# Kernel tuning notes

Hardware: AMD Instinct MI355X
Metric: run time of the kernel (lower is better)

## Reference

```python
import jax, jax.numpy as jnp
import numpy as np

OMEGA = 30.0

def _conv1x1(x, W, b):
    # x: [B, Cin, D, H, W]; W: [Cout, Cin]; b: [Cout]
    return jnp.einsum('oi,bidhw->bodhw', W, x) + b[None, :, None, None, None]

def setup_inputs() -> dict:
    key = jax.random.key(0)
    ks = jax.random.split(key, 12)
    B, D, H, Wd = 1, 8, 128, 128
    C = 256
    shp = (B, 3, D, H, Wd)
    std = np.sqrt(6.0 / C) / OMEGA
    return {
        'z': jax.random.normal(ks[0], shp, jnp.float32),
        'n': jax.random.normal(ks[1], shp, jnp.float32),
        'ad': jax.random.normal(ks[2], shp, jnp.float32),
        's': jax.random.normal(ks[3], shp, jnp.float32),
        'pixel_coords': jax.random.uniform(ks[4], shp, jnp.float32),
        'view_direction': jax.random.normal(ks[5], shp, jnp.float32),
        'W1': jax.random.normal(ks[6], (C, 12), jnp.float32) * std,
        'b1': jax.random.normal(ks[7], (C,), jnp.float32) * std,
        'W2': jax.random.normal(ks[8], (C, C), jnp.float32) * std,
        'b2': jax.random.normal(ks[9], (C,), jnp.float32) * std,
        'W4': jax.random.normal(ks[10], (3, C), jnp.float32) * 1e-4,
        'b4': jax.random.normal(ks[11], (3,), jnp.float32) * 1e-4,
    }

def reference(z, n, ad, s, pixel_coords, view_direction, W1, b1, W2, b2, W4, b4):
    # concat along channel dim: [B, 12, D, H, W]
    x = jnp.concatenate((s, n, pixel_coords, view_direction), axis=1)
    h = jnp.sin(OMEGA * _conv1x1(x, W1, b1))
    h = jnp.sin(OMEGA * _conv1x1(h, W2, b2))
    s_out = 0.5 * jnp.sin(OMEGA * _conv1x1(h, W4, b4))
    # lighting_predict_mode == 'total'
    return z + s_out
```

## Files before the change

kernel.cpp:

```cpp
#include <hip/hip_runtime.h>
#include <hip/hip_bf16.h>

#define NPIX (8*128*128)
#define CH   256
#define SCALE 4.774648292756860f

typedef __attribute__((ext_vector_type(8))) short bf16x8;
typedef __attribute__((ext_vector_type(4))) float f32x4;

__device__ inline unsigned int pkbf(float a, float b) {
    union { __hip_bfloat162 h; unsigned int u; } c;
    c.h = __float22bfloat162_rn(float2{a, b});
    return c.u;
}
__device__ inline unsigned short f2bf(float f) {
    unsigned int u = __float_as_uint(f);
    return (unsigned short)((u + 0x7FFFu + ((u >> 16) & 1u)) >> 16);
}
__device__ inline float sinrev(float t) {
    return __builtin_amdgcn_sinf(__builtin_amdgcn_fractf(t));
}
__device__ inline int kperm32(int k) {
    return (k & ~31) | ((k & 15) << 1) | ((k >> 4) & 1);
}

__global__ __launch_bounds__(256) void conv_weights(
    const float* __restrict__ W1, const float* __restrict__ W2,
    const float* __restrict__ W4,
    unsigned short* __restrict__ W2b, unsigned short* __restrict__ W1b,
    unsigned short* __restrict__ W4b)
{
    if (blockIdx.x < 256) {
        const int o = blockIdx.x, k = threadIdx.x;
        W2b[o*CH + kperm32(k)] = f2bf(W2[o*CH + k] * SCALE);
    } else {
        const int t = threadIdx.x;
        #pragma unroll
        for (int j = 0; j < 16; ++j)
            W1b[t*16 + j] = (j < 12) ? f2bf(W1[t*12 + j] * SCALE) : (unsigned short)0;
        const int kp = kperm32(t);
        #pragma unroll
        for (int r = 0; r < 16; ++r)
            W4b[r*CH + kp] = (r < 3) ? f2bf(W4[r*CH + t] * SCALE) : (unsigned short)0;
    }
}

template<bool PRE>
__global__ __launch_bounds__(512, 4) void rendernet5(
    const float* __restrict__ z,
    const float* __restrict__ nrm,
    const float* __restrict__ sph,
    const float* __restrict__ pc,
    const float* __restrict__ vd,
    const float* __restrict__ W1,
    const float* __restrict__ b1,
    const float* __restrict__ W2f,
    const unsigned short* __restrict__ W2b,
    const unsigned short* __restrict__ W1b,
    const float* __restrict__ b2,
    const float* __restrict__ W4f,
    const unsigned short* __restrict__ W4b,
    const float* __restrict__ b4,
    float* __restrict__ out)
{
    __shared__ __align__(16) char smem[64*512 + 64*80];
    char* xb = smem + 64*512;

    const int tid     = threadIdx.x;
    const int lane    = tid & 63;
    const int wave    = tid >> 6;
    const int lm      = lane & 15;
    const int lg      = lane >> 4;
    const int n0      = wave * 32;
    const int pixbase = blockIdx.x * 64;

    f32x4 acc[4][2];

    if constexpr (PRE) {
        {
            const int gp = pixbase + lane;
            unsigned int w0 = 0u, w1 = 0u;
            if (wave == 0) {
                w0 = pkbf(sph[0*NPIX+gp], sph[1*NPIX+gp]);
                w1 = pkbf(sph[2*NPIX+gp], nrm[0*NPIX+gp]);
            } else if (wave == 1) {
                w0 = pkbf(nrm[1*NPIX+gp], nrm[2*NPIX+gp]);
                w1 = pkbf(pc [0*NPIX+gp], pc [1*NPIX+gp]);
            } else if (wave == 2) {
                w0 = pkbf(pc[2*NPIX+gp], vd[0*NPIX+gp]);
                w1 = pkbf(vd[1*NPIX+gp], vd[2*NPIX+gp]);
            }
            *(unsigned int*)(xb + lane*80 + wave*8)     = w0;
            *(unsigned int*)(xb + lane*80 + wave*8 + 4) = w1;
        }
        __syncthreads();

        #pragma unroll
        for (int nf = 0; nf < 2; ++nf) {
            const float bv = b1[n0 + nf*16 + lm] * SCALE;
            #pragma unroll
            for (int mf = 0; mf < 4; ++mf) acc[mf][nf] = (f32x4){bv, bv, bv, bv};
        }

        bf16x8 w1f[2];
        #pragma unroll
        for (int nf = 0; nf < 2; ++nf) {
            bf16x8 t = *(const bf16x8*)(W1b + (n0 + nf*16 + lm)*16 + (lg & 1)*8);
            w1f[nf] = (lg < 2) ? t : (bf16x8){0,0,0,0,0,0,0,0};
        }
        bf16x8 ax[4];
        #pragma unroll
        for (int mf = 0; mf < 4; ++mf)
            ax[mf] = *(const bf16x8*)(xb + (mf*16 + lm)*80 + lg*16);

        #pragma unroll
        for (int nf = 0; nf < 2; ++nf)
            #pragma unroll
            for (int mf = 0; mf < 4; ++mf)
                acc[mf][nf] = __builtin_amdgcn_mfma_f32_16x16x32_bf16(
                                  ax[mf], w1f[nf], acc[mf][nf], 0, 0, 0);

        #pragma unroll
        for (int mf = 0; mf < 4; ++mf)
            #pragma unroll
            for (int r = 0; r < 4; ++r) {
                const int pix = mf*16 + lg*4 + r;
                const unsigned int pk = pkbf(sinrev(acc[mf][0][r]),
                                             sinrev(acc[mf][1][r]));
                *(unsigned int*)(smem + pix*512 + ((n0*2 + lm*4) ^ ((pix & 31) << 4))) = pk;
            }
    } else {
        const int gp = pixbase + lane;
        float xv[12];
        #pragma unroll
        for (int k = 0; k < 3; ++k) xv[k]     = sph[k*NPIX + gp];
        #pragma unroll
        for (int k = 0; k < 3; ++k) xv[3 + k] = nrm[k*NPIX + gp];
        #pragma unroll
        for (int k = 0; k < 3; ++k) xv[6 + k] = pc [k*NPIX + gp];
        #pragma unroll
        for (int k = 0; k < 3; ++k) xv[9 + k] = vd [k*NPIX + gp];
        #pragma unroll
        for (int c = 0; c < 32; ++c) {
            const int cc = n0 + c;
            float a = b1[cc];
            #pragma unroll
            for (int k = 0; k < 12; ++k) a += W1[cc*12 + k] * xv[k];
            const int kp = n0 + ((c & 15) << 1) + (c >> 4);
            *(unsigned short*)(smem + lane*512 + ((kp*2) ^ ((lane & 31) << 4))) =
                f2bf(__sinf(30.0f * a));
        }
    }
    __syncthreads();

    #pragma unroll
    for (int nf = 0; nf < 2; ++nf) {
        const float bv = PRE ? b2[n0 + nf*16 + lm] * SCALE : b2[n0 + nf*16 + lm];
        #pragma unroll
        for (int mf = 0; mf < 4; ++mf) acc[mf][nf] = (f32x4){bv, bv, bv, bv};
    }

    if constexpr (PRE) {
        const unsigned short* bp = W2b + (n0 + lm)*CH + lg*8;
        #pragma unroll
        for (int k0i = 0; k0i < 8; ++k0i) {
            bf16x8 bfr[2];
            #pragma unroll
            for (int nf = 0; nf < 2; ++nf)
                bfr[nf] = *(const bf16x8*)(bp + nf*16*CH + k0i*32);
            bf16x8 afr[4];
            #pragma unroll
            for (int mf = 0; mf < 4; ++mf) {
                const int pr = mf*16 + lm;
                afr[mf] = *(const bf16x8*)(smem + pr*512 +
                              ((k0i*64 + lg*16) ^ ((pr & 31) << 4)));
            }
            #pragma unroll
            for (int nf = 0; nf < 2; ++nf)
                #pragma unroll
                for (int mf = 0; mf < 4; ++mf)
                    acc[mf][nf] = __builtin_amdgcn_mfma_f32_16x16x32_bf16(
                                      afr[mf], bfr[nf], acc[mf][nf], 0, 0, 0);
        }
    } else {
        #pragma unroll
        for (int k0i = 0; k0i < 8; ++k0i) {
            bf16x8 afr[4];
            #pragma unroll
            for (int mf = 0; mf < 4; ++mf) {
                const int pr = mf*16 + lm;
                afr[mf] = *(const bf16x8*)(smem + pr*512 +
                              ((k0i*64 + lg*16) ^ ((pr & 31) << 4)));
            }
            #pragma unroll
            for (int nf = 0; nf < 2; ++nf) {
                bf16x8 t;
                #pragma unroll
                for (int j = 0; j < 8; ++j) {
                    const int kp = k0i*32 + lg*8 + j;
                    const int kr = (kp & ~31) | ((kp & 1) << 4) | ((kp >> 1) & 15);
                    t[j] = (short)f2bf(W2f[(n0 + nf*16 + lm)*CH + kr]);
                }
                #pragma unroll
                for (int mf = 0; mf < 4; ++mf)
                    acc[mf][nf] = __builtin_amdgcn_mfma_f32_16x16x32_bf16(
                                      afr[mf], t, acc[mf][nf], 0, 0, 0);
            }
        }
    }
    __syncthreads();

    #pragma unroll
    for (int mf = 0; mf < 4; ++mf)
        #pragma unroll
        for (int r = 0; r < 4; ++r) {
            const int pix = mf*16 + lg*4 + r;
            unsigned int pk;
            if constexpr (PRE)
                pk = pkbf(sinrev(acc[mf][0][r]), sinrev(acc[mf][1][r]));
            else
                pk = pkbf(__sinf(30.0f*acc[mf][0][r]), __sinf(30.0f*acc[mf][1][r]));
            *(unsigned int*)(smem + pix*512 + ((n0*2 + lm*4) ^ ((pix & 31) << 4))) = pk;
        }
    __syncthreads();

    if (wave == 0) {
        const float b4v = (lm < 3) ? (PRE ? b4[lm] * SCALE : b4[lm]) : 0.0f;
        f32x4 d[4];
        #pragma unroll
        for (int mf = 0; mf < 4; ++mf) d[mf] = (f32x4){b4v, b4v, b4v, b4v};

        #pragma unroll
        for (int k0i = 0; k0i < 8; ++k0i) {
            bf16x8 b4f;
            if constexpr (PRE) {
                b4f = *(const bf16x8*)(W4b + lm*CH + k0i*32 + lg*8);
            } else {
                #pragma unroll
                for (int j = 0; j < 8; ++j) {
                    const int kp = k0i*32 + lg*8 + j;
                    const int kr = (kp & ~31) | ((kp & 1) << 4) | ((kp >> 1) & 15);
                    b4f[j] = (lm < 3) ? (short)f2bf(W4f[lm*CH + kr]) : (short)0;
                }
            }
            bf16x8 afr[4];
            #pragma unroll
            for (int mf = 0; mf < 4; ++mf) {
                const int pr = mf*16 + lm;
                afr[mf] = *(const bf16x8*)(smem + pr*512 +
                              ((k0i*64 + lg*16) ^ ((pr & 31) << 4)));
            }
            #pragma unroll
            for (int mf = 0; mf < 4; ++mf)
                d[mf] = __builtin_amdgcn_mfma_f32_16x16x32_bf16(
                            afr[mf], b4f, d[mf], 0, 0, 0);
        }

        if (lm < 3) {
            #pragma unroll
            for (int mf = 0; mf < 4; ++mf)
                #pragma unroll
                for (int r = 0; r < 4; ++r) {
                    const int pix = mf*16 + lg*4 + r;
                    const int gi  = lm*NPIX + pixbase + pix;
                    const float sv = PRE ? sinrev(d[mf][r]) : __sinf(30.0f * d[mf][r]);
                    out[gi] = z[gi] + 0.5f * sv;
                }
        }
    }
}

extern "C" void kernel_launch(void* const* d_in, const int* in_sizes, int n_in,
                              void* d_out, int out_size, void* d_ws, size_t ws_size,
                              hipStream_t stream) {
    const float* z   = (const float*)d_in[0];
    const float* nrm = (const float*)d_in[1];
    const float* s   = (const float*)d_in[3];
    const float* pc  = (const float*)d_in[4];
    const float* vd  = (const float*)d_in[5];
    const float* W1  = (const float*)d_in[6];
    const float* b1  = (const float*)d_in[7];
    const float* W2  = (const float*)d_in[8];
    const float* b2  = (const float*)d_in[9];
    const float* W4  = (const float*)d_in[10];
    const float* b4  = (const float*)d_in[11];
    float* out = (float*)d_out;

    const size_t need = (size_t)(CH*CH + 16*CH + 16*CH) * sizeof(unsigned short);
    if (ws_size >= need) {
        unsigned short* W2b = (unsigned short*)d_ws;
        unsigned short* W1b = W2b + CH*CH;
        unsigned short* W4b = W1b + 16*CH;
        conv_weights<<<dim3(257), dim3(256), 0, stream>>>(W1, W2, W4, W2b, W1b, W4b);
        rendernet5<true><<<dim3(NPIX/64), dim3(512), 0, stream>>>(
            z, nrm, s, pc, vd, W1, b1, W2, W2b, W1b, b2, W4, W4b, b4, out);
    } else {
        rendernet5<false><<<dim3(NPIX/64), dim3(512), 0, stream>>>(
            z, nrm, s, pc, vd, W1, b1, W2, nullptr, nullptr, b2, W4, nullptr, b4, out);
    }
}
```

Baseline: 122.7 us.

## Widen block tile to 128 pixels with 2x4 wave grid over pixels and channels

Each block now handles 128 pixels instead of 64. The eight waves form a 2x4 grid, each computing a 64-pixel by 64-channel tile with 16 accumulators instead of 8. Every W2 fragment loaded from global memory now feeds twice as many MFMAs, which halves W2 traffic per pixel and the block count. In exchange, register pressure and LDS per block (about 74KB) both rise, which may reduce occupancy, and the final 3-channel projection now runs on two waves instead of one.

```diff
diff --git a/kernel.cpp b/kernel.cpp
--- a/kernel.cpp
+++ b/kernel.cpp
@@ -3,6 +3,7 @@
 
 #define NPIX (8*128*128)
 #define CH   256
+#define PPB  128
 #define SCALE 4.774648292756860f
 
 typedef __attribute__((ext_vector_type(8))) short bf16x8;
@@ -46,7 +47,7 @@
 }
 
 template<bool PRE>
-__global__ __launch_bounds__(512, 4) void rendernet5(
+__global__ __launch_bounds__(512, 4) void rendernet6(
     const float* __restrict__ z,
     const float* __restrict__ nrm,
     const float* __restrict__ sph,
@@ -63,58 +64,62 @@
     const float* __restrict__ b4,
     float* __restrict__ out)
 {
-    __shared__ __align__(16) char smem[64*512 + 64*80];
-    char* xb = smem + 64*512;
+    __shared__ __align__(16) char smem[PPB*512 + PPB*80];
+    char* xb = smem + PPB*512;
 
     const int tid     = threadIdx.x;
     const int lane    = tid & 63;
     const int wave    = tid >> 6;
+    const int wm      = wave >> 2;
+    const int wn      = wave & 3;
     const int lm      = lane & 15;
     const int lg      = lane >> 4;
-    const int n0      = wave * 32;
-    const int pixbase = blockIdx.x * 64;
-
-    f32x4 acc[4][2];
+    const int m0      = wm * 64;
+    const int n0      = wn * 64;
+    const int pixbase = blockIdx.x * PPB;
+
+    f32x4 acc[4][4];
 
     if constexpr (PRE) {
         {
-            const int gp = pixbase + lane;
-            unsigned int w0 = 0u, w1 = 0u;
-            if (wave == 0) {
-                w0 = pkbf(sph[0*NPIX+gp], sph[1*NPIX+gp]);
-                w1 = pkbf(sph[2*NPIX+gp], nrm[0*NPIX+gp]);
-            } else if (wave == 1) {
-                w0 = pkbf(nrm[1*NPIX+gp], nrm[2*NPIX+gp]);
-                w1 = pkbf(pc [0*NPIX+gp], pc [1*NPIX+gp]);
-            } else if (wave == 2) {
-                w0 = pkbf(pc[2*NPIX+gp], vd[0*NPIX+gp]);
-                w1 = pkbf(vd[1*NPIX+gp], vd[2*NPIX+gp]);
-            }
-            *(unsigned int*)(xb + lane*80 + wave*8)     = w0;
-            *(unsigned int*)(xb + lane*80 + wave*8 + 4) = w1;
+            const int p  = tid & 127;
+            const int sl = tid >> 7;
+            const int gp = pixbase + p;
+            union { unsigned int w[4]; bf16x8 v; } t;
+            t.w[0] = t.w[1] = t.w[2] = t.w[3] = 0u;
+            if (sl == 0) {
+                t.w[0] = pkbf(sph[0*NPIX+gp], sph[1*NPIX+gp]);
+                t.w[1] = pkbf(sph[2*NPIX+gp], nrm[0*NPIX+gp]);
+                t.w[2] = pkbf(nrm[1*NPIX+gp], nrm[2*NPIX+gp]);
+                t.w[3] = pkbf(pc [0*NPIX+gp], pc [1*NPIX+gp]);
+            } else if (sl == 1) {
+                t.w[0] = pkbf(pc[2*NPIX+gp], vd[0*NPIX+gp]);
+                t.w[1] = pkbf(vd[1*NPIX+gp], vd[2*NPIX+gp]);
+            }
+            *(bf16x8*)(xb + p*80 + sl*16) = t.v;
         }
         __syncthreads();
 
         #pragma unroll
-        for (int nf = 0; nf < 2; ++nf) {
+        for (int nf = 0; nf < 4; ++nf) {
             const float bv = b1[n0 + nf*16 + lm] * SCALE;
             #pragma unroll
             for (int mf = 0; mf < 4; ++mf) acc[mf][nf] = (f32x4){bv, bv, bv, bv};
         }
 
-        bf16x8 w1f[2];
-        #pragma unroll
-        for (int nf = 0; nf < 2; ++nf) {
+        bf16x8 w1f[4];
+        #pragma unroll
+        for (int nf = 0; nf < 4; ++nf) {
             bf16x8 t = *(const bf16x8*)(W1b + (n0 + nf*16 + lm)*16 + (lg & 1)*8);
             w1f[nf] = (lg < 2) ? t : (bf16x8){0,0,0,0,0,0,0,0};
         }
         bf16x8 ax[4];
         #pragma unroll
         for (int mf = 0; mf < 4; ++mf)
-            ax[mf] = *(const bf16x8*)(xb + (mf*16 + lm)*80 + lg*16);
-
-        #pragma unroll
-        for (int nf = 0; nf < 2; ++nf)
+            ax[mf] = *(const bf16x8*)(xb + (m0 + mf*16 + lm)*80 + lg*16);
+
+        #pragma unroll
+        for (int nf = 0; nf < 4; ++nf)
             #pragma unroll
             for (int mf = 0; mf < 4; ++mf)
                 acc[mf][nf] = __builtin_amdgcn_mfma_f32_16x16x32_bf16(
@@ -124,13 +129,17 @@
         for (int mf = 0; mf < 4; ++mf)
             #pragma unroll
             for (int r = 0; r < 4; ++r) {
-                const int pix = mf*16 + lg*4 + r;
-                const unsigned int pk = pkbf(sinrev(acc[mf][0][r]),
-                                             sinrev(acc[mf][1][r]));
-                *(unsigned int*)(smem + pix*512 + ((n0*2 + lm*4) ^ ((pix & 31) << 4))) = pk;
+                const int pix = m0 + mf*16 + lg*4 + r;
+                const int swz = (pix & 31) << 4;
+                *(unsigned int*)(smem + pix*512 + ((n0*2 + lm*4) ^ swz)) =
+                    pkbf(sinrev(acc[mf][0][r]), sinrev(acc[mf][1][r]));
+                *(unsigned int*)(smem + pix*512 + (((n0+32)*2 + lm*4) ^ swz)) =
+                    pkbf(sinrev(acc[mf][2][r]), sinrev(acc[mf][3][r]));
             }
     } else {
-        const int gp = pixbase + lane;
+        const int p  = tid & 127;
+        const int c0 = (tid >> 7) * 64;
+        const int gp = pixbase + p;
         float xv[12];
         #pragma unroll
         for (int k = 0; k < 3; ++k) xv[k]     = sph[k*NPIX + gp];
@@ -140,21 +149,20 @@
         for (int k = 0; k < 3; ++k) xv[6 + k] = pc [k*NPIX + gp];
         #pragma unroll
         for (int k = 0; k < 3; ++k) xv[9 + k] = vd [k*NPIX + gp];
-        #pragma unroll
-        for (int c = 0; c < 32; ++c) {
-            const int cc = n0 + c;
+        for (int c = 0; c < 64; ++c) {
+            const int cc = c0 + c;
             float a = b1[cc];
             #pragma unroll
             for (int k = 0; k < 12; ++k) a += W1[cc*12 + k] * xv[k];
-            const int kp = n0 + ((c & 15) << 1) + (c >> 4);
-            *(unsigned short*)(smem + lane*512 + ((kp*2) ^ ((lane & 31) << 4))) =
+            const int kp = kperm32(cc);
+            *(unsigned short*)(smem + p*512 + ((kp*2) ^ ((p & 31) << 4))) =
                 f2bf(__sinf(30.0f * a));
         }
     }
     __syncthreads();
 
     #pragma unroll
-    for (int nf = 0; nf < 2; ++nf) {
+    for (int nf = 0; nf < 4; ++nf) {
         const float bv = PRE ? b2[n0 + nf*16 + lm] * SCALE : b2[n0 + nf*16 + lm];
         #pragma unroll
         for (int mf = 0; mf < 4; ++mf) acc[mf][nf] = (f32x4){bv, bv, bv, bv};
@@ -164,19 +172,19 @@
         const unsigned short* bp = W2b + (n0 + lm)*CH + lg*8;
         #pragma unroll
         for (int k0i = 0; k0i < 8; ++k0i) {
-            bf16x8 bfr[2];
-            #pragma unroll
-            for (int nf = 0; nf < 2; ++nf)
+            bf16x8 bfr[4];
+            #pragma unroll
+            for (int nf = 0; nf < 4; ++nf)
                 bfr[nf] = *(const bf16x8*)(bp + nf*16*CH + k0i*32);
             bf16x8 afr[4];
             #pragma unroll
             for (int mf = 0; mf < 4; ++mf) {
-                const int pr = mf*16 + lm;
+                const int pr = m0 + mf*16 + lm;
                 afr[mf] = *(const bf16x8*)(smem + pr*512 +
                               ((k0i*64 + lg*16) ^ ((pr & 31) << 4)));
             }
             #pragma unroll
-            for (int nf = 0; nf < 2; ++nf)
+            for (int nf = 0; nf < 4; ++nf)
                 #pragma unroll
                 for (int mf = 0; mf < 4; ++mf)
                     acc[mf][nf] = __builtin_amdgcn_mfma_f32_16x16x32_bf16(
@@ -188,12 +196,12 @@
             bf16x8 afr[4];
             #pragma unroll
             for (int mf = 0; mf < 4; ++mf) {
-                const int pr = mf*16 + lm;
+                const int pr = m0 + mf*16 + lm;
                 afr[mf] = *(const bf16x8*)(smem + pr*512 +
                               ((k0i*64 + lg*16) ^ ((pr & 31) << 4)));
             }
             #pragma unroll
-            for (int nf = 0; nf < 2; ++nf) {
+            for (int nf = 0; nf < 4; ++nf) {
                 bf16x8 t;
                 #pragma unroll
                 for (int j = 0; j < 8; ++j) {
@@ -214,17 +222,22 @@
     for (int mf = 0; mf < 4; ++mf)
         #pragma unroll
         for (int r = 0; r < 4; ++r) {
-            const int pix = mf*16 + lg*4 + r;
-            unsigned int pk;
-            if constexpr (PRE)
-                pk = pkbf(sinrev(acc[mf][0][r]), sinrev(acc[mf][1][r]));
-            else
-                pk = pkbf(__sinf(30.0f*acc[mf][0][r]), __sinf(30.0f*acc[mf][1][r]));
-            *(unsigned int*)(smem + pix*512 + ((n0*2 + lm*4) ^ ((pix & 31) << 4))) = pk;
+            const int pix = m0 + mf*16 + lg*4 + r;
+            const int swz = (pix & 31) << 4;
+            unsigned int pk0, pk1;
+            if constexpr (PRE) {
+                pk0 = pkbf(sinrev(acc[mf][0][r]), sinrev(acc[mf][1][r]));
+                pk1 = pkbf(sinrev(acc[mf][2][r]), sinrev(acc[mf][3][r]));
+            } else {
+                pk0 = pkbf(__sinf(30.0f*acc[mf][0][r]), __sinf(30.0f*acc[mf][1][r]));
+                pk1 = pkbf(__sinf(30.0f*acc[mf][2][r]), __sinf(30.0f*acc[mf][3][r]));
+            }
+            *(unsigned int*)(smem + pix*512 + ((n0*2 + lm*4) ^ swz))      = pk0;
+            *(unsigned int*)(smem + pix*512 + (((n0+32)*2 + lm*4) ^ swz)) = pk1;
         }
     __syncthreads();
 
-    if (wave == 0) {
+    if (wn == 0) {
         const float b4v = (lm < 3) ? (PRE ? b4[lm] * SCALE : b4[lm]) : 0.0f;
         f32x4 d[4];
         #pragma unroll
@@ -246,7 +259,7 @@
             bf16x8 afr[4];
             #pragma unroll
             for (int mf = 0; mf < 4; ++mf) {
-                const int pr = mf*16 + lm;
+                const int pr = m0 + mf*16 + lm;
                 afr[mf] = *(const bf16x8*)(smem + pr*512 +
                               ((k0i*64 + lg*16) ^ ((pr & 31) << 4)));
             }
@@ -261,7 +274,7 @@
             for (int mf = 0; mf < 4; ++mf)
                 #pragma unroll
                 for (int r = 0; r < 4; ++r) {
-                    const int pix = mf*16 + lg*4 + r;
+                    const int pix = m0 + mf*16 + lg*4 + r;
                     const int gi  = lm*NPIX + pixbase + pix;
                     const float sv = PRE ? sinrev(d[mf][r]) : __sinf(30.0f * d[mf][r]);
                     out[gi] = z[gi] + 0.5f * sv;
@@ -292,10 +305,10 @@
         unsigned short* W1b = W2b + CH*CH;
         unsigned short* W4b = W1b + 16*CH;
         conv_weights<<<dim3(257), dim3(256), 0, stream>>>(W1, W2, W4, W2b, W1b, W4b);
-        rendernet5<true><<<dim3(NPIX/64), dim3(512), 0, stream>>>(
+        rendernet6<true><<<dim3(NPIX/PPB), dim3(512), 0, stream>>>(
             z, nrm, s, pc, vd, W1, b1, W2, W2b, W1b, b2, W4, W4b, b4, out);
     } else {
-        rendernet5<false><<<dim3(NPIX/64), dim3(512), 0, stream>>>(
+        rendernet6<false><<<dim3(NPIX/PPB), dim3(512), 0, stream>>>(
             z, nrm, s, pc, vd, W1, b1, W2, nullptr, nullptr, b2, W4, nullptr, b4, out);
     }
 }
```

Result: slower. 139.9 us (+14.0%).
